# Kernel tuning notes

Measured on AMD Instinct MI355X. Metric: run time of the kernel, lower is better.

The kernel has to match this reference:

```python
import jax, jax.numpy as jnp
import numpy as np

SCALE = 2.0   # init scale
OFFSET = 0.5  # init offset
BIG = 1e10    # stand-in for +inf so grads stay finite
N_PAD = 2048  # number of zero-padded pc columns per sample


def setup_inputs() -> dict:
    key = jax.random.key(0)
    k1, k2 = jax.random.split(key)
    vertices = jax.random.normal(k1, (4, 3, 64, 32, 64), dtype=jnp.float32)
    pc = jax.random.normal(k2, (4, 3, 8192), dtype=jnp.float32)
    # zero-pad the tail columns, mimicking variable-length point clouds
    pc = pc.at[:, :, 8192 - N_PAD:].set(0.0)
    return {"vertices": vertices, "pc": pc}


def _chamfer_loss(v, p, mask):
    # v: [N,3] mesh-top points; p: [M,3] cloud points; mask: [M] valid flags
    # squared pairwise distances via ||v||^2 + ||p||^2 - 2 v.p
    d = (jnp.sum(v * v, axis=1)[:, None]
         + jnp.sum(p * p, axis=1)[None, :]
         - 2.0 * (v @ p.T))                      # [N, M]
    dist1 = jnp.min(jnp.where(mask[None, :], d, BIG), axis=1)  # [N] v -> nearest valid p
    dist2 = jnp.min(d, axis=0)                                  # [M] p -> nearest v
    n_valid = jnp.maximum(jnp.sum(mask), 1).astype(d.dtype)
    return jnp.mean(dist1) + jnp.sum(jnp.where(mask, dist2, 0.0)) / n_valid


def reference(vertices, pc):
    B = vertices.shape[0]
    # top surface: last index along dim 3, flattened -> [B, 3, N]
    top = vertices[:, :, :, -1, :].reshape(B, 3, -1)
    top = (top - OFFSET) * SCALE
    v = jnp.transpose(top, (0, 2, 1))   # [B, N, 3]
    p = jnp.transpose(pc, (0, 2, 1))    # [B, M, 3]
    mask = ~jnp.all(pc == 0.0, axis=1)  # [B, M] valid (non-zero-padded) points
    loss = jax.vmap(_chamfer_loss)(v, p, mask)  # [B]
    return jnp.mean(loss)
```

## Files before the change

kernel.cpp:

```cpp
#include <hip/hip_runtime.h>

#define BATCH   4
#define NPTS    4096
#define MPTS    8192
#define TPB     256
#define VPT     8
#define MSPLIT  32
#define NSPLIT  16
#define MLEN    (MPTS / MSPLIT)
#define NLEN    (NPTS / NSPLIT)
#define D1_NBLK (NPTS / (TPB * VPT))
#define D2_MBLK (MPTS / (TPB * VPT))
#define D1_BLOCKS (BATCH * D1_NBLK * MSPLIT)
#define D2_BLOCKS (BATCH * D2_MBLK * NSPLIT)
#define BIGF    1.0e30f

#define PART1_ELEMS (MSPLIT * BATCH * NPTS)
#define PART2_ELEMS (NSPLIT * BATCH * MPTS)

#define R1_BLOCKS ((BATCH * NPTS) / (TPB * 4))
#define R2_BLOCKS ((BATCH * MPTS) / (TPB * 4))
#define R_BLOCKS  (R1_BLOCKS + R2_BLOCKS)

#define CTRL_FLOATS 16

__device__ __forceinline__ float vtop(const float* __restrict__ v, int b, int c, int n) {
    return v[b * 393216 + c * 131072 + ((n >> 6) << 11) + 1984 + (n & 63)];
}

__global__ void __launch_bounds__(TPB) dist_kernel(const float* __restrict__ vert,
                                                   const float* __restrict__ pc,
                                                   float* __restrict__ part1,
                                                   float* __restrict__ part2,
                                                   float* __restrict__ ctrl) {
    __shared__ float4 tile[TPB];
    const int tid = threadIdx.x;
    int blk = blockIdx.x;

    if (blk == 0 && tid < CTRL_FLOATS) ctrl[tid] = 0.0f;

    if (blk < D1_BLOCKS) {
        const int c  = blk % MSPLIT;
        const int nb = (blk / MSPLIT) % D1_NBLK;
        const int b  = blk / (MSPLIT * D1_NBLK);
        const float* pcb = pc + (size_t)b * 3 * MPTS;

        {
            const int m = c * MLEN + tid;
            const float qx = pcb[m], qy = pcb[MPTS + m], qz = pcb[2 * MPTS + m];
            const bool valid = !(qx == 0.0f && qy == 0.0f && qz == 0.0f);
            const float qn2 = valid ? 0.5f * (qx * qx + qy * qy + qz * qz) : BIGF;
            tile[tid] = make_float4(qx, qy, qz, qn2);
        }

        float vx[VPT], vy[VPT], vz[VPT], best[VPT];
        const int nbase = nb * (TPB * VPT) + tid;
#pragma unroll
        for (int k = 0; k < VPT; ++k) {
            const int n = nbase + k * TPB;
            vx[k] = (vtop(vert, b, 0, n) - 0.5f) * 2.0f;
            vy[k] = (vtop(vert, b, 1, n) - 0.5f) * 2.0f;
            vz[k] = (vtop(vert, b, 2, n) - 0.5f) * 2.0f;
            best[k] = BIGF;
        }
        __syncthreads();

#pragma unroll 4
        for (int j = 0; j < MLEN; ++j) {
            const float4 q = tile[j];
#pragma unroll
            for (int k = 0; k < VPT; ++k) {
                best[k] = fminf(best[k],
                    fmaf(-vx[k], q.x, fmaf(-vy[k], q.y, fmaf(-vz[k], q.z, q.w))));
            }
        }

        float* outp = part1 + (size_t)c * (BATCH * NPTS) + (size_t)b * NPTS;
#pragma unroll
        for (int k = 0; k < VPT; ++k) {
            const int n = nbase + k * TPB;
            const float vv = vx[k]*vx[k] + vy[k]*vy[k] + vz[k]*vz[k];
            outp[n] = fmaxf(vv + 2.0f * best[k], 0.0f);
        }
    } else {
        blk -= D1_BLOCKS;
        const int c  = blk % NSPLIT;
        const int mb = (blk / NSPLIT) % D2_MBLK;
        const int b  = blk / (NSPLIT * D2_MBLK);
        const float* pcb = pc + (size_t)b * 3 * MPTS;

        {
            const int n = c * NLEN + tid;
            const float sx = (vtop(vert, b, 0, n) - 0.5f) * 2.0f;
            const float sy = (vtop(vert, b, 1, n) - 0.5f) * 2.0f;
            const float sz = (vtop(vert, b, 2, n) - 0.5f) * 2.0f;
            tile[tid] = make_float4(sx, sy, sz, 0.5f * (sx*sx + sy*sy + sz*sz));
        }

        float qx[VPT], qy[VPT], qz[VPT], best[VPT];
        const int mbase = mb * (TPB * VPT) + tid;
#pragma unroll
        for (int k = 0; k < VPT; ++k) {
            const int m = mbase + k * TPB;
            qx[k] = pcb[m];
            qy[k] = pcb[MPTS + m];
            qz[k] = pcb[2 * MPTS + m];
            best[k] = BIGF;
        }
        __syncthreads();

#pragma unroll 4
        for (int j = 0; j < NLEN; ++j) {
            const float4 t = tile[j];
#pragma unroll
            for (int k = 0; k < VPT; ++k) {
                best[k] = fminf(best[k],
                    fmaf(-qx[k], t.x, fmaf(-qy[k], t.y, fmaf(-qz[k], t.z, t.w))));
            }
        }

        float* outp = part2 + (size_t)c * (BATCH * MPTS) + (size_t)b * MPTS;
#pragma unroll
        for (int k = 0; k < VPT; ++k) {
            const int m = mbase + k * TPB;
            const float qq = qx[k]*qx[k] + qy[k]*qy[k] + qz[k]*qz[k];
            outp[m] = fmaxf(qq + 2.0f * best[k], 0.0f);
        }
    }
}

__global__ void __launch_bounds__(TPB) reduce_kernel(const float* __restrict__ part1,
                                                     const float* __restrict__ part2,
                                                     const float* __restrict__ pc,
                                                     float* __restrict__ ctrl,
                                                     float* __restrict__ out) {
    const int tid = threadIdx.x;
    const int wid = tid >> 6;
    __shared__ float rs[4], rc[4];

    float s = 0.0f, cn = 0.0f;
    int b;

    if (blockIdx.x < R1_BLOCKS) {
        const int gid = blockIdx.x * (TPB * 4) + tid * 4;
        b = gid / NPTS;
        float4 best = make_float4(BIGF, BIGF, BIGF, BIGF);
#pragma unroll
        for (int c = 0; c < MSPLIT; ++c) {
            const float4 v = *(const float4*)&part1[(size_t)c * (BATCH * NPTS) + gid];
            best.x = fminf(best.x, v.x); best.y = fminf(best.y, v.y);
            best.z = fminf(best.z, v.z); best.w = fminf(best.w, v.w);
        }
        s = best.x + best.y + best.z + best.w;
    } else {
        const int g2 = (blockIdx.x - R1_BLOCKS) * (TPB * 4) + tid * 4;
        b = g2 / MPTS;
        const int m = g2 % MPTS;
        float4 best = make_float4(BIGF, BIGF, BIGF, BIGF);
#pragma unroll
        for (int c = 0; c < NSPLIT; ++c) {
            const float4 v = *(const float4*)&part2[(size_t)c * (BATCH * MPTS) + g2];
            best.x = fminf(best.x, v.x); best.y = fminf(best.y, v.y);
            best.z = fminf(best.z, v.z); best.w = fminf(best.w, v.w);
        }
        const float* pcb = pc + (size_t)b * 3 * MPTS;
        const float4 qx = *(const float4*)&pcb[m];
        const float4 qy = *(const float4*)&pcb[MPTS + m];
        const float4 qz = *(const float4*)&pcb[2 * MPTS + m];
        const bool v0 = !(qx.x == 0.0f && qy.x == 0.0f && qz.x == 0.0f);
        const bool v1 = !(qx.y == 0.0f && qy.y == 0.0f && qz.y == 0.0f);
        const bool v2 = !(qx.z == 0.0f && qy.z == 0.0f && qz.z == 0.0f);
        const bool v3 = !(qx.w == 0.0f && qy.w == 0.0f && qz.w == 0.0f);
        s  = (v0 ? best.x : 0.0f) + (v1 ? best.y : 0.0f)
           + (v2 ? best.z : 0.0f) + (v3 ? best.w : 0.0f);
        cn = (float)v0 + (float)v1 + (float)v2 + (float)v3;
    }

    for (int off = 32; off > 0; off >>= 1) {
        s  += __shfl_down(s, off, 64);
        cn += __shfl_down(cn, off, 64);
    }
    if ((tid & 63) == 0) { rs[wid] = s; rc[wid] = cn; }
    __syncthreads();

    if (tid == 0) {
        const float ts = rs[0] + rs[1] + rs[2] + rs[3];
        if (blockIdx.x < R1_BLOCKS) {
            atomicAdd(&ctrl[b], ts);
        } else {
            atomicAdd(&ctrl[4 + b], ts);
            atomicAdd(&ctrl[8 + b], rc[0] + rc[1] + rc[2] + rc[3]);
        }
        __threadfence();
        const unsigned int old = atomicAdd((unsigned int*)&ctrl[15], 1u);
        if (old == R_BLOCKS - 1) {
            float t = 0.0f;
            for (int bb = 0; bb < BATCH; ++bb) {
                const float s1 = atomicAdd(&ctrl[bb], 0.0f);
                const float s2 = atomicAdd(&ctrl[4 + bb], 0.0f);
                const float nv = atomicAdd(&ctrl[8 + bb], 0.0f);
                t += s1 * (1.0f / (float)NPTS) + s2 / fmaxf(nv, 1.0f);
            }
            out[0] = t * (1.0f / (float)BATCH);
        }
    }
}

extern "C" void kernel_launch(void* const* d_in, const int* in_sizes, int n_in,
                              void* d_out, int out_size, void* d_ws, size_t ws_size,
                              hipStream_t stream) {
    const float* vert = (const float*)d_in[0];
    const float* pc   = (const float*)d_in[1];
    float* out = (float*)d_out;

    float* part1 = (float*)d_ws;
    float* part2 = part1 + PART1_ELEMS;
    float* ctrl  = part2 + PART2_ELEMS;

    dist_kernel<<<D1_BLOCKS + D2_BLOCKS, TPB, 0, stream>>>(vert, pc, part1, part2, ctrl);
    reduce_kernel<<<R_BLOCKS, TPB, 0, stream>>>(part1, part2, pc, ctrl, out);
}
```

Before: 87.20 us.

## Precompute packed point arrays, skip all-padded chunks, and double split counts

Adds a pre-pass kernel that packs transformed mesh-top points and cloud points into float4 arrays with half squared norms, with padded cloud points flagged via a large weight. The distance kernel now reads these packed arrays directly from global memory instead of staging shared tiles. It also uses block-wide counts to skip chunks whose cloud points are all padding. Split counts are doubled for more blocks and shorter inner loops. The reduce kernel is simplified to one point per thread. The trade-off is an extra launch, larger partial buffers for the reduction to read, and uniform global loads in place of LDS.

```diff
diff --git a/kernel.cpp b/kernel.cpp
--- a/kernel.cpp
+++ b/kernel.cpp
@@ -5,8 +5,8 @@
 #define MPTS    8192
 #define TPB     256
 #define VPT     8
-#define MSPLIT  32
-#define NSPLIT  16
+#define MSPLIT  64
+#define NSPLIT  32
 #define MLEN    (MPTS / MSPLIT)
 #define NLEN    (NPTS / NSPLIT)
 #define D1_NBLK (NPTS / (TPB * VPT))
@@ -17,9 +17,11 @@
 
 #define PART1_ELEMS (MSPLIT * BATCH * NPTS)
 #define PART2_ELEMS (NSPLIT * BATCH * MPTS)
-
-#define R1_BLOCKS ((BATCH * NPTS) / (TPB * 4))
-#define R2_BLOCKS ((BATCH * MPTS) / (TPB * 4))
+#define VQ_POINTS   (BATCH * NPTS)
+#define PQ_POINTS   (BATCH * MPTS)
+
+#define R1_BLOCKS ((BATCH * NPTS) / TPB)
+#define R2_BLOCKS ((BATCH * MPTS) / TPB)
 #define R_BLOCKS  (R1_BLOCKS + R2_BLOCKS)
 
 #define CTRL_FLOATS 16
@@ -28,110 +30,124 @@
     return v[b * 393216 + c * 131072 + ((n >> 6) << 11) + 1984 + (n & 63)];
 }
 
-__global__ void __launch_bounds__(TPB) dist_kernel(const float* __restrict__ vert,
-                                                   const float* __restrict__ pc,
+__global__ void __launch_bounds__(TPB) pre_kernel(const float* __restrict__ vert,
+                                                  const float* __restrict__ pc,
+                                                  float4* __restrict__ vq,
+                                                  float4* __restrict__ pq,
+                                                  float* __restrict__ ctrl) {
+    const int g = blockIdx.x * TPB + threadIdx.x;
+    if (g < CTRL_FLOATS) ctrl[g] = 0.0f;
+    if (g < VQ_POINTS) {
+        const int b = g >> 12, n = g & (NPTS - 1);
+        const float sx = (vtop(vert, b, 0, n) - 0.5f) * 2.0f;
+        const float sy = (vtop(vert, b, 1, n) - 0.5f) * 2.0f;
+        const float sz = (vtop(vert, b, 2, n) - 0.5f) * 2.0f;
+        vq[g] = make_float4(sx, sy, sz, 0.5f * (sx * sx + sy * sy + sz * sz));
+    } else {
+        const int h = g - VQ_POINTS;
+        const int b = h >> 13, m = h & (MPTS - 1);
+        const float* pcb = pc + (size_t)b * 3 * MPTS;
+        const float qx = pcb[m], qy = pcb[MPTS + m], qz = pcb[2 * MPTS + m];
+        const bool valid = !(qx == 0.0f && qy == 0.0f && qz == 0.0f);
+        const float w = valid ? 0.5f * (qx * qx + qy * qy + qz * qz) : BIGF;
+        pq[h] = make_float4(qx, qy, qz, w);
+    }
+}
+
+__global__ void __launch_bounds__(TPB) dist_kernel(const float4* __restrict__ vq,
+                                                   const float4* __restrict__ pq,
                                                    float* __restrict__ part1,
-                                                   float* __restrict__ part2,
-                                                   float* __restrict__ ctrl) {
-    __shared__ float4 tile[TPB];
+                                                   float* __restrict__ part2) {
     const int tid = threadIdx.x;
     int blk = blockIdx.x;
-
-    if (blk == 0 && tid < CTRL_FLOATS) ctrl[tid] = 0.0f;
 
     if (blk < D1_BLOCKS) {
         const int c  = blk % MSPLIT;
         const int nb = (blk / MSPLIT) % D1_NBLK;
         const int b  = blk / (MSPLIT * D1_NBLK);
-        const float* pcb = pc + (size_t)b * 3 * MPTS;
-
-        {
-            const int m = c * MLEN + tid;
-            const float qx = pcb[m], qy = pcb[MPTS + m], qz = pcb[2 * MPTS + m];
-            const bool valid = !(qx == 0.0f && qy == 0.0f && qz == 0.0f);
-            const float qn2 = valid ? 0.5f * (qx * qx + qy * qy + qz * qz) : BIGF;
-            tile[tid] = make_float4(qx, qy, qz, qn2);
-        }
-
-        float vx[VPT], vy[VPT], vz[VPT], best[VPT];
+        const float4* __restrict__ qp = pq + b * MPTS + c * MLEN;
         const int nbase = nb * (TPB * VPT) + tid;
+        float* __restrict__ outp = part1 + (size_t)c * (BATCH * NPTS) + (size_t)b * NPTS;
+
+        const bool av = (tid < MLEN) && (qp[tid].w != BIGF);
+        if (__syncthreads_count(av) == 0) {
+#pragma unroll
+            for (int k = 0; k < VPT; ++k) outp[nbase + k * TPB] = BIGF;
+            return;
+        }
+
+        float vx[VPT], vy[VPT], vz[VPT], vv[VPT], best[VPT];
+        const float4* __restrict__ vp = vq + b * NPTS;
 #pragma unroll
         for (int k = 0; k < VPT; ++k) {
-            const int n = nbase + k * TPB;
-            vx[k] = (vtop(vert, b, 0, n) - 0.5f) * 2.0f;
-            vy[k] = (vtop(vert, b, 1, n) - 0.5f) * 2.0f;
-            vz[k] = (vtop(vert, b, 2, n) - 0.5f) * 2.0f;
+            const float4 t = vp[nbase + k * TPB];
+            vx[k] = t.x; vy[k] = t.y; vz[k] = t.z;
+            vv[k] = 2.0f * t.w;
             best[k] = BIGF;
         }
-        __syncthreads();
-
-#pragma unroll 4
-        for (int j = 0; j < MLEN; ++j) {
-            const float4 q = tile[j];
+
+#pragma unroll 2
+        for (int j = 0; j < MLEN; j += 2) {
+            const float4 qa = qp[j];
+            const float4 qb = qp[j + 1];
 #pragma unroll
             for (int k = 0; k < VPT; ++k) {
-                best[k] = fminf(best[k],
-                    fmaf(-vx[k], q.x, fmaf(-vy[k], q.y, fmaf(-vz[k], q.z, q.w))));
+                const float ea = fmaf(-vx[k], qa.x, fmaf(-vy[k], qa.y, fmaf(-vz[k], qa.z, qa.w)));
+                const float eb = fmaf(-vx[k], qb.x, fmaf(-vy[k], qb.y, fmaf(-vz[k], qb.z, qb.w)));
+                best[k] = fminf(best[k], fminf(ea, eb));
             }
         }
 
-        float* outp = part1 + (size_t)c * (BATCH * NPTS) + (size_t)b * NPTS;
-#pragma unroll
-        for (int k = 0; k < VPT; ++k) {
-            const int n = nbase + k * TPB;
-            const float vv = vx[k]*vx[k] + vy[k]*vy[k] + vz[k]*vz[k];
-            outp[n] = fmaxf(vv + 2.0f * best[k], 0.0f);
-        }
+#pragma unroll
+        for (int k = 0; k < VPT; ++k)
+            outp[nbase + k * TPB] = fmaxf(fmaf(2.0f, best[k], vv[k]), 0.0f);
     } else {
         blk -= D1_BLOCKS;
         const int c  = blk % NSPLIT;
         const int mb = (blk / NSPLIT) % D2_MBLK;
         const int b  = blk / (NSPLIT * D2_MBLK);
-        const float* pcb = pc + (size_t)b * 3 * MPTS;
-
-        {
-            const int n = c * NLEN + tid;
-            const float sx = (vtop(vert, b, 0, n) - 0.5f) * 2.0f;
-            const float sy = (vtop(vert, b, 1, n) - 0.5f) * 2.0f;
-            const float sz = (vtop(vert, b, 2, n) - 0.5f) * 2.0f;
-            tile[tid] = make_float4(sx, sy, sz, 0.5f * (sx*sx + sy*sy + sz*sz));
-        }
+        const float4* __restrict__ vp = vq + b * NPTS + c * NLEN;
+        const float4* __restrict__ qp = pq + b * MPTS;
+        const int mbase = mb * (TPB * VPT) + tid;
+        float* __restrict__ outp = part2 + (size_t)c * (BATCH * MPTS) + (size_t)b * MPTS;
 
         float qx[VPT], qy[VPT], qz[VPT], best[VPT];
-        const int mbase = mb * (TPB * VPT) + tid;
+        bool anyv = false;
 #pragma unroll
         for (int k = 0; k < VPT; ++k) {
-            const int m = mbase + k * TPB;
-            qx[k] = pcb[m];
-            qy[k] = pcb[MPTS + m];
-            qz[k] = pcb[2 * MPTS + m];
-            best[k] = BIGF;
-        }
-        __syncthreads();
-
-#pragma unroll 4
-        for (int j = 0; j < NLEN; ++j) {
-            const float4 t = tile[j];
+            const float4 t = qp[mbase + k * TPB];
+            qx[k] = t.x; qy[k] = t.y; qz[k] = t.z; best[k] = BIGF;
+            anyv = anyv || (t.w != BIGF);
+        }
+        if (__syncthreads_count(anyv) == 0) {
+#pragma unroll
+            for (int k = 0; k < VPT; ++k) outp[mbase + k * TPB] = 0.0f;
+            return;
+        }
+
+#pragma unroll 2
+        for (int j = 0; j < NLEN; j += 2) {
+            const float4 ta = vp[j];
+            const float4 tb = vp[j + 1];
 #pragma unroll
             for (int k = 0; k < VPT; ++k) {
-                best[k] = fminf(best[k],
-                    fmaf(-qx[k], t.x, fmaf(-qy[k], t.y, fmaf(-qz[k], t.z, t.w))));
+                const float ea = fmaf(-qx[k], ta.x, fmaf(-qy[k], ta.y, fmaf(-qz[k], ta.z, ta.w)));
+                const float eb = fmaf(-qx[k], tb.x, fmaf(-qy[k], tb.y, fmaf(-qz[k], tb.z, tb.w)));
+                best[k] = fminf(best[k], fminf(ea, eb));
             }
         }
 
-        float* outp = part2 + (size_t)c * (BATCH * MPTS) + (size_t)b * MPTS;
 #pragma unroll
         for (int k = 0; k < VPT; ++k) {
-            const int m = mbase + k * TPB;
             const float qq = qx[k]*qx[k] + qy[k]*qy[k] + qz[k]*qz[k];
-            outp[m] = fmaxf(qq + 2.0f * best[k], 0.0f);
+            outp[mbase + k * TPB] = fmaxf(fmaf(2.0f, best[k], qq), 0.0f);
         }
     }
 }
 
 __global__ void __launch_bounds__(TPB) reduce_kernel(const float* __restrict__ part1,
                                                      const float* __restrict__ part2,
-                                                     const float* __restrict__ pc,
+                                                     const float4* __restrict__ pq,
                                                      float* __restrict__ ctrl,
                                                      float* __restrict__ out) {
     const int tid = threadIdx.x;
@@ -142,38 +158,23 @@
     int b;
 
     if (blockIdx.x < R1_BLOCKS) {
-        const int gid = blockIdx.x * (TPB * 4) + tid * 4;
-        b = gid / NPTS;
-        float4 best = make_float4(BIGF, BIGF, BIGF, BIGF);
-#pragma unroll
-        for (int c = 0; c < MSPLIT; ++c) {
-            const float4 v = *(const float4*)&part1[(size_t)c * (BATCH * NPTS) + gid];
-            best.x = fminf(best.x, v.x); best.y = fminf(best.y, v.y);
-            best.z = fminf(best.z, v.z); best.w = fminf(best.w, v.w);
-        }
-        s = best.x + best.y + best.z + best.w;
+        const int gid = blockIdx.x * TPB + tid;
+        b = gid >> 12;
+        float best = BIGF;
+#pragma unroll 8
+        for (int c = 0; c < MSPLIT; ++c)
+            best = fminf(best, part1[(size_t)c * (BATCH * NPTS) + gid]);
+        s = best;
     } else {
-        const int g2 = (blockIdx.x - R1_BLOCKS) * (TPB * 4) + tid * 4;
-        b = g2 / MPTS;
-        const int m = g2 % MPTS;
-        float4 best = make_float4(BIGF, BIGF, BIGF, BIGF);
-#pragma unroll
-        for (int c = 0; c < NSPLIT; ++c) {
-            const float4 v = *(const float4*)&part2[(size_t)c * (BATCH * MPTS) + g2];
-            best.x = fminf(best.x, v.x); best.y = fminf(best.y, v.y);
-            best.z = fminf(best.z, v.z); best.w = fminf(best.w, v.w);
-        }
-        const float* pcb = pc + (size_t)b * 3 * MPTS;
-        const float4 qx = *(const float4*)&pcb[m];
-        const float4 qy = *(const float4*)&pcb[MPTS + m];
-        const float4 qz = *(const float4*)&pcb[2 * MPTS + m];
-        const bool v0 = !(qx.x == 0.0f && qy.x == 0.0f && qz.x == 0.0f);
-        const bool v1 = !(qx.y == 0.0f && qy.y == 0.0f && qz.y == 0.0f);
-        const bool v2 = !(qx.z == 0.0f && qy.z == 0.0f && qz.z == 0.0f);
-        const bool v3 = !(qx.w == 0.0f && qy.w == 0.0f && qz.w == 0.0f);
-        s  = (v0 ? best.x : 0.0f) + (v1 ? best.y : 0.0f)
-           + (v2 ? best.z : 0.0f) + (v3 ? best.w : 0.0f);
-        cn = (float)v0 + (float)v1 + (float)v2 + (float)v3;
+        const int g2 = (blockIdx.x - R1_BLOCKS) * TPB + tid;
+        b = g2 >> 13;
+        float best = BIGF;
+#pragma unroll 8
+        for (int c = 0; c < NSPLIT; ++c)
+            best = fminf(best, part2[(size_t)c * (BATCH * MPTS) + g2]);
+        const bool v = (pq[g2].w != BIGF);
+        s  = v ? best : 0.0f;
+        cn = v ? 1.0f : 0.0f;
     }
 
     for (int off = 32; off > 0; off >>= 1) {
@@ -215,8 +216,11 @@
 
     float* part1 = (float*)d_ws;
     float* part2 = part1 + PART1_ELEMS;
-    float* ctrl  = part2 + PART2_ELEMS;
-
-    dist_kernel<<<D1_BLOCKS + D2_BLOCKS, TPB, 0, stream>>>(vert, pc, part1, part2, ctrl);
-    reduce_kernel<<<R_BLOCKS, TPB, 0, stream>>>(part1, part2, pc, ctrl, out);
-}
+    float4* vq   = (float4*)(part2 + PART2_ELEMS);
+    float4* pq   = vq + VQ_POINTS;
+    float* ctrl  = (float*)(pq + PQ_POINTS);
+
+    pre_kernel<<<(VQ_POINTS + PQ_POINTS) / TPB, TPB, 0, stream>>>(vert, pc, vq, pq, ctrl);
+    dist_kernel<<<D1_BLOCKS + D2_BLOCKS, TPB, 0, stream>>>(vq, pq, part1, part2);
+    reduce_kernel<<<R_BLOCKS, TPB, 0, stream>>>(part1, part2, pq, ctrl, out);
+}
```

Result: slower. 107.3 us (+23.0%).

## Skip all-padding point tiles at block level and restructure inner min loops

Applied to the files above, without the earlier changes.

Each distance block uses __syncthreads_count to detect whether its cloud tile or query points are entirely zero-padded and exits early. For part1 it writes the sentinel value; for part2 it writes nothing, because the reduction masks those entries out. The inner loops now handle two tile entries per iteration and merge them with a paired fminf to shorten the min dependency chain. The reduction kernel moves from float4 per thread to one element per thread across four times as many blocks. The skip depends on padding being aligned to whole tiles, and the scalar reduction gives up vectorised loads.

```diff
diff --git a/kernel.cpp b/kernel.cpp
--- a/kernel.cpp
+++ b/kernel.cpp
@@ -18,8 +18,8 @@
 #define PART1_ELEMS (MSPLIT * BATCH * NPTS)
 #define PART2_ELEMS (NSPLIT * BATCH * MPTS)
 
-#define R1_BLOCKS ((BATCH * NPTS) / (TPB * 4))
-#define R2_BLOCKS ((BATCH * MPTS) / (TPB * 4))
+#define R1_BLOCKS ((BATCH * NPTS) / TPB)
+#define R2_BLOCKS ((BATCH * MPTS) / TPB)
 #define R_BLOCKS  (R1_BLOCKS + R2_BLOCKS)
 
 #define CTRL_FLOATS 16
@@ -44,17 +44,25 @@
         const int nb = (blk / MSPLIT) % D1_NBLK;
         const int b  = blk / (MSPLIT * D1_NBLK);
         const float* pcb = pc + (size_t)b * 3 * MPTS;
-
+        const int nbase = nb * (TPB * VPT) + tid;
+        float* __restrict__ outp = part1 + (size_t)c * (BATCH * NPTS) + (size_t)b * NPTS;
+
+        bool valid;
         {
             const int m = c * MLEN + tid;
             const float qx = pcb[m], qy = pcb[MPTS + m], qz = pcb[2 * MPTS + m];
-            const bool valid = !(qx == 0.0f && qy == 0.0f && qz == 0.0f);
+            valid = !(qx == 0.0f && qy == 0.0f && qz == 0.0f);
             const float qn2 = valid ? 0.5f * (qx * qx + qy * qy + qz * qz) : BIGF;
             tile[tid] = make_float4(qx, qy, qz, qn2);
         }
 
+        if (__syncthreads_count(valid) == 0) {
+#pragma unroll
+            for (int k = 0; k < VPT; ++k) outp[nbase + k * TPB] = BIGF;
+            return;
+        }
+
         float vx[VPT], vy[VPT], vz[VPT], best[VPT];
-        const int nbase = nb * (TPB * VPT) + tid;
 #pragma unroll
         for (int k = 0; k < VPT; ++k) {
             const int n = nbase + k * TPB;
@@ -63,24 +71,23 @@
             vz[k] = (vtop(vert, b, 2, n) - 0.5f) * 2.0f;
             best[k] = BIGF;
         }
-        __syncthreads();
-
-#pragma unroll 4
-        for (int j = 0; j < MLEN; ++j) {
-            const float4 q = tile[j];
+
+#pragma unroll 2
+        for (int j = 0; j < MLEN; j += 2) {
+            const float4 qa = tile[j];
+            const float4 qb = tile[j + 1];
 #pragma unroll
             for (int k = 0; k < VPT; ++k) {
-                best[k] = fminf(best[k],
-                    fmaf(-vx[k], q.x, fmaf(-vy[k], q.y, fmaf(-vz[k], q.z, q.w))));
+                const float ea = fmaf(-vx[k], qa.x, fmaf(-vy[k], qa.y, fmaf(-vz[k], qa.z, qa.w)));
+                const float eb = fmaf(-vx[k], qb.x, fmaf(-vy[k], qb.y, fmaf(-vz[k], qb.z, qb.w)));
+                best[k] = fminf(best[k], fminf(ea, eb));
             }
         }
 
-        float* outp = part1 + (size_t)c * (BATCH * NPTS) + (size_t)b * NPTS;
-#pragma unroll
-        for (int k = 0; k < VPT; ++k) {
-            const int n = nbase + k * TPB;
+#pragma unroll
+        for (int k = 0; k < VPT; ++k) {
             const float vv = vx[k]*vx[k] + vy[k]*vy[k] + vz[k]*vz[k];
-            outp[n] = fmaxf(vv + 2.0f * best[k], 0.0f);
+            outp[nbase + k * TPB] = fmaxf(fmaf(2.0f, best[k], vv), 0.0f);
         }
     } else {
         blk -= D1_BLOCKS;
@@ -88,6 +95,8 @@
         const int mb = (blk / NSPLIT) % D2_MBLK;
         const int b  = blk / (NSPLIT * D2_MBLK);
         const float* pcb = pc + (size_t)b * 3 * MPTS;
+        const int mbase = mb * (TPB * VPT) + tid;
+        float* __restrict__ outp = part2 + (size_t)c * (BATCH * MPTS) + (size_t)b * MPTS;
 
         {
             const int n = c * NLEN + tid;
@@ -98,7 +107,7 @@
         }
 
         float qx[VPT], qy[VPT], qz[VPT], best[VPT];
-        const int mbase = mb * (TPB * VPT) + tid;
+        bool anyv = false;
 #pragma unroll
         for (int k = 0; k < VPT; ++k) {
             const int m = mbase + k * TPB;
@@ -106,25 +115,26 @@
             qy[k] = pcb[MPTS + m];
             qz[k] = pcb[2 * MPTS + m];
             best[k] = BIGF;
-        }
-        __syncthreads();
-
-#pragma unroll 4
-        for (int j = 0; j < NLEN; ++j) {
-            const float4 t = tile[j];
+            anyv = anyv || !(qx[k] == 0.0f && qy[k] == 0.0f && qz[k] == 0.0f);
+        }
+        if (__syncthreads_count(anyv) == 0) return;
+
+#pragma unroll 2
+        for (int j = 0; j < NLEN; j += 2) {
+            const float4 ta = tile[j];
+            const float4 tb = tile[j + 1];
 #pragma unroll
             for (int k = 0; k < VPT; ++k) {
-                best[k] = fminf(best[k],
-                    fmaf(-qx[k], t.x, fmaf(-qy[k], t.y, fmaf(-qz[k], t.z, t.w))));
+                const float ea = fmaf(-qx[k], ta.x, fmaf(-qy[k], ta.y, fmaf(-qz[k], ta.z, ta.w)));
+                const float eb = fmaf(-qx[k], tb.x, fmaf(-qy[k], tb.y, fmaf(-qz[k], tb.z, tb.w)));
+                best[k] = fminf(best[k], fminf(ea, eb));
             }
         }
 
-        float* outp = part2 + (size_t)c * (BATCH * MPTS) + (size_t)b * MPTS;
-#pragma unroll
-        for (int k = 0; k < VPT; ++k) {
-            const int m = mbase + k * TPB;
+#pragma unroll
+        for (int k = 0; k < VPT; ++k) {
             const float qq = qx[k]*qx[k] + qy[k]*qy[k] + qz[k]*qz[k];
-            outp[m] = fmaxf(qq + 2.0f * best[k], 0.0f);
+            outp[mbase + k * TPB] = fmaxf(fmaf(2.0f, best[k], qq), 0.0f);
         }
     }
 }
@@ -142,38 +152,28 @@
     int b;
 
     if (blockIdx.x < R1_BLOCKS) {
-        const int gid = blockIdx.x * (TPB * 4) + tid * 4;
-        b = gid / NPTS;
-        float4 best = make_float4(BIGF, BIGF, BIGF, BIGF);
-#pragma unroll
-        for (int c = 0; c < MSPLIT; ++c) {
-            const float4 v = *(const float4*)&part1[(size_t)c * (BATCH * NPTS) + gid];
-            best.x = fminf(best.x, v.x); best.y = fminf(best.y, v.y);
-            best.z = fminf(best.z, v.z); best.w = fminf(best.w, v.w);
-        }
-        s = best.x + best.y + best.z + best.w;
+        const int gid = blockIdx.x * TPB + tid;
+        b = gid >> 12;
+        float best = BIGF;
+#pragma unroll
+        for (int c = 0; c < MSPLIT; c += 2)
+            best = fminf(best, fminf(part1[(size_t)c * (BATCH * NPTS) + gid],
+                                     part1[(size_t)(c + 1) * (BATCH * NPTS) + gid]));
+        s = best;
     } else {
-        const int g2 = (blockIdx.x - R1_BLOCKS) * (TPB * 4) + tid * 4;
-        b = g2 / MPTS;
-        const int m = g2 % MPTS;
-        float4 best = make_float4(BIGF, BIGF, BIGF, BIGF);
-#pragma unroll
-        for (int c = 0; c < NSPLIT; ++c) {
-            const float4 v = *(const float4*)&part2[(size_t)c * (BATCH * MPTS) + g2];
-            best.x = fminf(best.x, v.x); best.y = fminf(best.y, v.y);
-            best.z = fminf(best.z, v.z); best.w = fminf(best.w, v.w);
-        }
+        const int g2 = (blockIdx.x - R1_BLOCKS) * TPB + tid;
+        b = g2 >> 13;
+        const int m = g2 & (MPTS - 1);
+        float best = BIGF;
+#pragma unroll
+        for (int c = 0; c < NSPLIT; c += 2)
+            best = fminf(best, fminf(part2[(size_t)c * (BATCH * MPTS) + g2],
+                                     part2[(size_t)(c + 1) * (BATCH * MPTS) + g2]));
         const float* pcb = pc + (size_t)b * 3 * MPTS;
-        const float4 qx = *(const float4*)&pcb[m];
-        const float4 qy = *(const float4*)&pcb[MPTS + m];
-        const float4 qz = *(const float4*)&pcb[2 * MPTS + m];
-        const bool v0 = !(qx.x == 0.0f && qy.x == 0.0f && qz.x == 0.0f);
-        const bool v1 = !(qx.y == 0.0f && qy.y == 0.0f && qz.y == 0.0f);
-        const bool v2 = !(qx.z == 0.0f && qy.z == 0.0f && qz.z == 0.0f);
-        const bool v3 = !(qx.w == 0.0f && qy.w == 0.0f && qz.w == 0.0f);
-        s  = (v0 ? best.x : 0.0f) + (v1 ? best.y : 0.0f)
-           + (v2 ? best.z : 0.0f) + (v3 ? best.w : 0.0f);
-        cn = (float)v0 + (float)v1 + (float)v2 + (float)v3;
+        const float qx = pcb[m], qy = pcb[MPTS + m], qz = pcb[2 * MPTS + m];
+        const bool v = !(qx == 0.0f && qy == 0.0f && qz == 0.0f);
+        s  = v ? best : 0.0f;
+        cn = v ? 1.0f : 0.0f;
     }
 
     for (int off = 32; off > 0; off >>= 1) {
```

After: 89.37 us. 1.02x slower.
